# Optimization experiments

Measured on AMD Instinct MI355X. Metric: run time of the kernel, lower is better.

## Reference

```python
import jax, jax.numpy as jnp
import numpy as np

B, H, L, D = 8, 8, 2048, 64
FACTOR = 5


def _num_sel(length):
    return min(int(FACTOR * np.ceil(np.log(length))), length)


def setup_inputs() -> dict:
    key = jax.random.key(0)
    kq, kk, kv, ki = jax.random.split(key, 4)
    num_k = _num_sel(L)
    return {
        "q": jax.random.normal(kq, (B, H, L, D), dtype=jnp.float32),
        "k": jax.random.normal(kk, (B, H, L, D), dtype=jnp.float32),
        "v": jax.random.normal(kv, (B, H, L, D), dtype=jnp.float32),
        "random_index": jax.random.randint(ki, (L, num_k), 0, L, dtype=jnp.int32),
    }


def reference(q, k, v, random_index):
    b, h, q_len, d = q.shape
    k_len = k.shape[2]
    num_q = _num_sel(q_len)

    # --- random K sampling per query: k_s[b,h,i,j,:] = k[b,h,random_index[i,j],:]
    k_s = k[:, :, random_index, :]                      # (B,H,L,num_k,D)
    pre_attn = jnp.einsum('bhid,bhijd->bhij', q, k_s)   # (B,H,L,num_k)
    measure = pre_attn.max(-1) - pre_attn.sum(-1) / k_len  # (B,H,L)

    # --- top-k query selection (sorted=False in torch; order-insensitive math)
    _, idx = jax.lax.top_k(measure, num_q)              # (B,H,num_q)
    q_sel = jnp.take_along_axis(q, idx[..., None], axis=2)  # (B,H,num_q,D)

    # --- reduced attention over all keys
    attn = jnp.einsum('bhid,bhjd->bhij', q_sel, k) * (d ** -0.5)  # (B,H,num_q,k_len)

    # ProbMask: causal mask per selected query index (mask where j > idx[i])
    mask = jnp.arange(k_len)[None, None, None, :] > idx[..., None]
    attn = jnp.where(mask, -jnp.inf, attn)
    attn = jax.nn.softmax(attn, axis=-1)

    out_sel = jnp.einsum('bhij,bhjd->bhid', attn, v)    # (B,H,num_q,D)

    # --- context initialization (use_mask=True branch) and scatter back
    context = jnp.cumsum(v, axis=2)                     # (B,H,L,D)
    bi = jnp.arange(b)[:, None, None]
    hi = jnp.arange(h)[None, :, None]
    out = context.at[bi, hi, idx].set(out_sel)          # (B,H,L,D)
    return out, attn
```

## Files before the change

### kernel.cpp

```cpp
#include <hip/hip_runtime.h>
#include <float.h>
#include <math.h>

#define B_  8
#define H_  8
#define L_  2048
#define D_  64
#define NS  40
#define BH  (B_*H_)
#define SCALE 0.125f


template<int CTRL>
__device__ __forceinline__ float dpp_add(float x) {
    int s = __builtin_amdgcn_update_dpp(0, __float_as_int(x), CTRL, 0xF, 0xF, true);
    return x + __int_as_float(s);
}

__global__ __launch_bounds__(256) void measure_kernel(
    const float* __restrict__ q, const float* __restrict__ k,
    const int* __restrict__ ridx, float* __restrict__ measure)
{
    int wave = threadIdx.x >> 6, lane = threadIdx.x & 63;
    int b = blockIdx.x;
    int xcd = b & 7, s = b >> 3;
    int bh  = xcd + ((s >> 9) << 3);
    int i   = (s & 511) * 4 + wave;
    int oct = lane >> 3;
    int e   = lane & 7;

    int4 r4 = *(const int4*)(ridx + i * NS + oct * 4);
    int  r5 = ridx[i * NS + 32 + oct];
    int rr[5] = { r4.x, r4.y, r4.z, r4.w, r5 };

    const float4* kb = (const float4*)(k + (size_t)bh * L_ * D_);
    const float4* qp = (const float4*)(q + ((size_t)bh * L_ + i) * D_);
    float4 qa = qp[e];
    float4 qb = qp[e + 8];

    float mx = -FLT_MAX, sm = 0.f;
    #pragma unroll
    for (int p = 0; p < 5; ++p) {
        int base = rr[p] << 4;
        float4 ka = kb[base + e];
        float4 kc = kb[base + 8 + e];
        float pa = qa.x*ka.x + qa.y*ka.y + qa.z*ka.z + qa.w*ka.w;
        float pb = qb.x*kc.x + qb.y*kc.y + qb.z*kc.z + qb.w*kc.w;
        float pp = pa + pb;
        pp = dpp_add<0x111>(pp);
        pp = dpp_add<0x112>(pp);
        pp = dpp_add<0x114>(pp);
        mx = fmaxf(mx, pp);
        sm += pp;
    }
    mx = fmaxf(mx, __shfl_xor(mx,  8, 64));  sm += __shfl_xor(sm,  8, 64);
    mx = fmaxf(mx, __shfl_xor(mx, 16, 64));  sm += __shfl_xor(sm, 16, 64);
    mx = fmaxf(mx, __shfl_xor(mx, 32, 64));  sm += __shfl_xor(sm, 32, 64);
    if (lane == 7)
        measure[(size_t)bh * L_ + i] = mx - sm * (1.0f / (float)L_);
}

__global__ __launch_bounds__(256) void topk_kernel(
    const float* __restrict__ measure, int* __restrict__ idxOut)
{
    __shared__ float wv[4]; __shared__ int wi[4];
    __shared__ float bvS;   __shared__ int biS;
    int b = blockIdx.x;
    int bh = (b & 7) + ((b >> 3) << 3);
    int t = threadIdx.x;
    const float4* m4 = (const float4*)(measure + (size_t)bh * L_);
    float vals[8];
    float4 a = m4[t*2], bb = m4[t*2 + 1];
    vals[0]=a.x; vals[1]=a.y; vals[2]=a.z; vals[3]=a.w;
    vals[4]=bb.x; vals[5]=bb.y; vals[6]=bb.z; vals[7]=bb.w;

    float lv = -FLT_MAX; int li = t*8;
    #pragma unroll
    for (int e = 0; e < 8; ++e) if (vals[e] > lv) { lv = vals[e]; li = t*8 + e; }

    int lane = t & 63, w = t >> 6;
    for (int r = 0; r < NS; ++r) {
        float v = lv; int idx = li;
        #pragma unroll
        for (int off = 32; off; off >>= 1) {
            float ov = __shfl_xor(v, off, 64);
            int   oi = __shfl_xor(idx, off, 64);
            if (ov > v || (ov == v && oi < idx)) { v = ov; idx = oi; }
        }
        if (lane == 0) { wv[w] = v; wi[w] = idx; }
        __syncthreads();
        if (t == 0) {
            float bv = wv[0]; int bi = wi[0];
            #pragma unroll
            for (int ww = 1; ww < 4; ++ww)
                if (wv[ww] > bv || (wv[ww] == bv && wi[ww] < bi)) { bv = wv[ww]; bi = wi[ww]; }
            bvS = bv; biS = bi;
            idxOut[bh * NS + r] = bi;
        }
        __syncthreads();
        int bi = biS;
        if ((bi >> 3) == t) {
            #pragma unroll
            for (int e = 0; e < 8; ++e) if ((bi & 7) == e) vals[e] = -FLT_MAX;
            lv = -FLT_MAX; li = t*8;
            #pragma unroll
            for (int e = 0; e < 8; ++e) if (vals[e] > lv) { lv = vals[e]; li = t*8 + e; }
        }
        __syncthreads();
    }
}

__global__ __launch_bounds__(256) void cumsum_fused(
    const float* __restrict__ v, float* __restrict__ out)
{
    __shared__ float4 part[64][5];
    int b = blockIdx.x;
    int xcd = b & 7, s = b >> 3;
    int bh  = xcd + ((s >> 2) << 3);
    int cg  = s & 3;
    int col = threadIdx.x & 3, sub = threadIdx.x >> 2;
    int c0 = cg*4 + col;
    int r0 = sub * 32;
    const float4* vb = (const float4*)(v + (size_t)bh * L_ * D_);
    float4*       ob = (float4*)(out + (size_t)bh * L_ * D_);

    float4 acc = make_float4(0,0,0,0);
    #pragma unroll
    for (int r = 0; r < 32; ++r) {
        float4 x = vb[(size_t)(r0 + r)*16 + c0];
        acc.x += x.x; acc.y += x.y; acc.z += x.z; acc.w += x.w;
    }
    part[sub][col] = acc;
    __syncthreads();

    float4 run = make_float4(0,0,0,0);
    for (int cc = 0; cc < sub; ++cc) {
        float4 x = part[cc][col];
        run.x += x.x; run.y += x.y; run.z += x.z; run.w += x.w;
    }

    #pragma unroll
    for (int r = 0; r < 32; ++r) {
        float4 x = vb[(size_t)(r0 + r)*16 + c0];
        run.x += x.x; run.y += x.y; run.z += x.z; run.w += x.w;
        ob[(size_t)(r0 + r)*16 + c0] = run;
    }
}

__global__ __launch_bounds__(256) void scores_kernel(
    const float* __restrict__ q, const float* __restrict__ k,
    const int* __restrict__ idxSel, float* __restrict__ attn)
{
    __shared__ float4 kbuf[16 * 129];
    int b = blockIdx.x;
    int xcd = b & 7, s = b >> 3;
    int bh  = xcd + ((s / 10) << 3);
    int grp = s % 10;
    int qi = threadIdx.x >> 6, sub = threadIdx.x & 63;
    int rank = grp*4 + qi;
    int qrow = idxSel[bh*NS + rank];

    const float4* qrp = (const float4*)(q + ((size_t)bh * L_ + qrow) * D_);
    float4 qreg[16];
    #pragma unroll
    for (int g = 0; g < 16; ++g) qreg[g] = qrp[g];

    const float4* kb = (const float4*)(k + (size_t)bh * L_ * D_);
    float sc0[16], sc1[16];

    #pragma unroll
    for (int c = 0; c < 16; ++c) {
        __syncthreads();
        int j0 = c * 128;
        #pragma unroll
        for (int it = 0; it < 8; ++it) {
            int fi = threadIdx.x + 256*it;
            int g = fi & 15, j = fi >> 4;
            kbuf[g*129 + j] = kb[(size_t)(j0 + j)*16 + g];
        }
        __syncthreads();
        float acc0 = 0.f, acc1 = 0.f;
        #pragma unroll
        for (int g = 0; g < 16; ++g) {
            float4 k0 = kbuf[g*129 + sub];
            float4 k1 = kbuf[g*129 + sub + 64];
            float4 qq = qreg[g];
            acc0 += qq.x*k0.x + qq.y*k0.y + qq.z*k0.z + qq.w*k0.w;
            acc1 += qq.x*k1.x + qq.y*k1.y + qq.z*k1.z + qq.w*k1.w;
        }
        sc0[c] = acc0 * SCALE;
        sc1[c] = acc1 * SCALE;
    }

    float mx = -FLT_MAX;
    #pragma unroll
    for (int c = 0; c < 16; ++c) {
        if (c*128 + sub      <= qrow) mx = fmaxf(mx, sc0[c]);
        if (c*128 + sub + 64 <= qrow) mx = fmaxf(mx, sc1[c]);
    }
    #pragma unroll
    for (int off = 32; off; off >>= 1) mx = fmaxf(mx, __shfl_xor(mx, off, 64));

    float sum = 0.f;
    #pragma unroll
    for (int c = 0; c < 16; ++c) {
        sc0[c] = (c*128 + sub      <= qrow) ? __expf(sc0[c] - mx) : 0.f;
        sc1[c] = (c*128 + sub + 64 <= qrow) ? __expf(sc1[c] - mx) : 0.f;
        sum += sc0[c] + sc1[c];
    }
    #pragma unroll
    for (int off = 32; off; off >>= 1) sum += __shfl_xor(sum, off, 64);
    float inv = 1.f / sum;

    float* arow = attn + (size_t)(bh*NS + rank) * L_;
    #pragma unroll
    for (int c = 0; c < 16; ++c) {
        arow[c*128 + sub]      = sc0[c] * inv;
        arow[c*128 + sub + 64] = sc1[c] * inv;
    }
}

__global__ __launch_bounds__(256) void pv_kernel(
    const float* __restrict__ v, const int* __restrict__ idxSel,
    const float* __restrict__ attn, float* __restrict__ out)
{
    __shared__ float wl[4][L_ + 64];
    __shared__ float4 part[16][16];
    __shared__ int qr4[4];
    int b = blockIdx.x;
    int xcd = b & 7, s = b >> 3;
    int bh  = xcd + ((s / 10) << 3);
    int grp = s % 10;
    int t = threadIdx.x;
    if (t < 4) qr4[t] = idxSel[bh*NS + grp*4 + t];

    #pragma unroll
    for (int it = 0; it < 8; ++it) {
        int f = t + 256*it;
        int rr = f >> 9, fi = f & 511;
        const float4* ar = (const float4*)(attn + (size_t)(bh*NS + grp*4 + rr) * L_);
        float4 x = ar[fi];
        int j = 4*fi;
        *((float4*)&wl[rr][j + 4*(j >> 7)]) = x;
    }
    __syncthreads();

    int maxq = max(max(qr4[0], qr4[1]), max(qr4[2], qr4[3]));
    int d4 = t & 15, seg = t >> 4;
    const float4* vb = (const float4*)(v + (size_t)bh * L_ * D_);
    float4 acc[4];
    #pragma unroll
    for (int rr = 0; rr < 4; ++rr) acc[rr] = make_float4(0,0,0,0);

    int jlo = seg*128, jhi = min(jlo + 127, maxq);
    for (int j = jlo; j <= jhi; ++j) {
        float4 x = vb[(size_t)j*16 + d4];
        int jp = j + 4*(j >> 7);
        #pragma unroll
        for (int rr = 0; rr < 4; ++rr) {
            float wgt = wl[rr][jp];
            acc[rr].x += wgt*x.x; acc[rr].y += wgt*x.y;
            acc[rr].z += wgt*x.z; acc[rr].w += wgt*x.w;
        }
    }

    #pragma unroll
    for (int rr = 0; rr < 4; ++rr) {
        part[seg][d4] = acc[rr];
        __syncthreads();
        float4 a = acc[rr];
        for (int s2 = 8; s2; s2 >>= 1) {
            if (seg < s2) {
                float4 o = part[seg + s2][d4];
                a.x += o.x; a.y += o.y; a.z += o.z; a.w += o.w;
                part[seg][d4] = a;
            }
            __syncthreads();
        }
        if (seg == 0) {
            float4* orow = (float4*)(out + ((size_t)bh * L_ + qr4[rr]) * D_);
            orow[d4] = a;
        }
        __syncthreads();
    }
}

extern "C" void kernel_launch(void* const* d_in, const int* in_sizes, int n_in,
                              void* d_out, int out_size, void* d_ws, size_t ws_size,
                              hipStream_t stream) {
    const float* q    = (const float*)d_in[0];
    const float* k    = (const float*)d_in[1];
    const float* v    = (const float*)d_in[2];
    const int*   ridx = (const int*)d_in[3];

    float* out     = (float*)d_out;
    float* attnOut = out + (size_t)BH * L_ * D_;

    float*  measure = (float*)d_ws;
    int*    idxSel  = (int*)((char*)d_ws + (size_t)BH * L_ * sizeof(float));

    measure_kernel<<<BH * L_ / 4, 256, 0, stream>>>(q, k, ridx, measure);
    topk_kernel   <<<BH,          256, 0, stream>>>(measure, idxSel);
    cumsum_fused  <<<BH * 4,      256, 0, stream>>>(v, out);
    scores_kernel <<<BH * 10,     256, 0, stream>>>(q, k, idxSel, attnOut);
    pv_kernel     <<<BH * 10,     256, 0, stream>>>(v, idxSel, attnOut, out);
}
```

Before: 325.9 us.

## Restructure top-k as per-wave local top-40 then 4-way merge

After: 325.0 us. No clear change (-0.3%).

```diff
diff --git a/kernel.cpp b/kernel.cpp
--- a/kernel.cpp
+++ b/kernel.cpp
@@ -63,22 +63,24 @@
 __global__ __launch_bounds__(256) void topk_kernel(
     const float* __restrict__ measure, int* __restrict__ idxOut)
 {
-    __shared__ float wv[4]; __shared__ int wi[4];
-    __shared__ float bvS;   __shared__ int biS;
-    int b = blockIdx.x;
-    int bh = (b & 7) + ((b >> 3) << 3);
-    int t = threadIdx.x;
+    __shared__ float segVal[4][NS];
+    __shared__ int   segIdx[4][NS];
+    int bh = blockIdx.x;
+    int t = threadIdx.x, w = t >> 6, lane = t & 63;
     const float4* m4 = (const float4*)(measure + (size_t)bh * L_);
+
     float vals[8];
-    float4 a = m4[t*2], bb = m4[t*2 + 1];
-    vals[0]=a.x; vals[1]=a.y; vals[2]=a.z; vals[3]=a.w;
+    float4 a  = m4[128*w + 2*lane];
+    float4 bb = m4[128*w + 2*lane + 1];
+    vals[0]=a.x;  vals[1]=a.y;  vals[2]=a.z;  vals[3]=a.w;
     vals[4]=bb.x; vals[5]=bb.y; vals[6]=bb.z; vals[7]=bb.w;
-
-    float lv = -FLT_MAX; int li = t*8;
-    #pragma unroll
-    for (int e = 0; e < 8; ++e) if (vals[e] > lv) { lv = vals[e]; li = t*8 + e; }
-
-    int lane = t & 63, w = t >> 6;
+    int gbase = 512*w + 8*lane;
+
+    float lv = -FLT_MAX; int li = 0x7fffffff;
+    #pragma unroll
+    for (int e = 0; e < 8; ++e)
+        if (vals[e] > lv) { lv = vals[e]; li = gbase + e; }
+
     for (int r = 0; r < NS; ++r) {
         float v = lv; int idx = li;
         #pragma unroll
@@ -87,26 +89,36 @@
             int   oi = __shfl_xor(idx, off, 64);
             if (ov > v || (ov == v && oi < idx)) { v = ov; idx = oi; }
         }
-        if (lane == 0) { wv[w] = v; wi[w] = idx; }
-        __syncthreads();
-        if (t == 0) {
-            float bv = wv[0]; int bi = wi[0];
+        if (lane == 0) { segVal[w][r] = v; segIdx[w][r] = idx; }
+        if (((idx >> 3) & 63) == lane) {
+            int slot = idx & 7;
             #pragma unroll
-            for (int ww = 1; ww < 4; ++ww)
-                if (wv[ww] > bv || (wv[ww] == bv && wi[ww] < bi)) { bv = wv[ww]; bi = wi[ww]; }
-            bvS = bv; biS = bi;
-            idxOut[bh * NS + r] = bi;
-        }
-        __syncthreads();
-        int bi = biS;
-        if ((bi >> 3) == t) {
+            for (int e = 0; e < 8; ++e) if (e == slot) vals[e] = -FLT_MAX;
+            lv = -FLT_MAX; li = 0x7fffffff;
             #pragma unroll
-            for (int e = 0; e < 8; ++e) if ((bi & 7) == e) vals[e] = -FLT_MAX;
-            lv = -FLT_MAX; li = t*8;
-            #pragma unroll
-            for (int e = 0; e < 8; ++e) if (vals[e] > lv) { lv = vals[e]; li = t*8 + e; }
-        }
-        __syncthreads();
+            for (int e = 0; e < 8; ++e)
+                if (vals[e] > lv) { lv = vals[e]; li = gbase + e; }
+        }
+    }
+    __syncthreads();
+
+    if (w == 0) {
+        int s = lane & 3;
+        int h = 0;
+        float hv = segVal[s][0]; int hi_ = segIdx[s][0];
+        for (int r = 0; r < NS; ++r) {
+            float v = hv; int idx = hi_; int ws = s;
+            float ov = __shfl_xor(v, 1, 64); int oi = __shfl_xor(idx, 1, 64); int os = __shfl_xor(ws, 1, 64);
+            if (ov > v || (ov == v && oi < idx)) { v = ov; idx = oi; ws = os; }
+            ov = __shfl_xor(v, 2, 64); oi = __shfl_xor(idx, 2, 64); os = __shfl_xor(ws, 2, 64);
+            if (ov > v || (ov == v && oi < idx)) { v = ov; idx = oi; ws = os; }
+            if (lane == 0) idxOut[bh*NS + r] = idx;
+            if (s == ws) {
+                ++h;
+                if (h < NS) { hv = segVal[s][h]; hi_ = segIdx[s][h]; }
+                else        { hv = -FLT_MAX;     hi_ = 0x7fffffff;  }
+            }
+        }
     }
 }
 
```
